# Performance work log

Hardware: AMD Instinct MI355X
Metric: run time of the kernel (lower is better)

The kernel has to match this reference:

```python
import jax, jax.numpy as jnp
import numpy as np

N = 50000      # nodes
E = 800000     # edges (avg degree 16)
D_IN, D_H, D_OUT = 128, 256, 128


def setup_inputs() -> dict:
    key = jax.random.key(0)
    ks = jax.random.split(key, 8)
    x = jax.random.normal(ks[0], (N, D_IN), dtype=jnp.float32)
    edge_index = jax.random.randint(ks[1], (2, E), 0, N, dtype=jnp.int64)
    s1 = 1.0 / np.sqrt(D_IN).astype(np.float32)
    s2 = 1.0 / np.sqrt(D_H).astype(np.float32)
    return {
        "x": x,
        "edge_index": edge_index,
        "W1l": jax.random.normal(ks[2], (D_H, D_IN), jnp.float32) * s1,
        "b1l": jnp.zeros((D_H,), jnp.float32),
        "W1r": jax.random.normal(ks[3], (D_H, D_IN), jnp.float32) * s1,
        "W2l": jax.random.normal(ks[4], (D_OUT, D_H), jnp.float32) * s2,
        "b2l": jnp.zeros((D_OUT,), jnp.float32),
        "W2r": jax.random.normal(ks[5], (D_OUT, D_H), jnp.float32) * s2,
    }


def sage_conv(x, src, dst, Wl, bl, Wr):
    # mean-aggregate source features into destination nodes
    agg = jax.ops.segment_sum(x[src], dst, num_segments=N)           # [N, d_in]
    deg = jax.ops.segment_sum(jnp.ones((src.shape[0],), x.dtype), dst, num_segments=N)
    mean = agg / jnp.maximum(deg, 1.0)[:, None]
    # lin_l(mean_agg) + lin_r(x_root); lin_r has no bias (PyG SAGEConv default)
    return mean @ Wl.T + bl + x @ Wr.T


def reference(x, edge_index, W1l, b1l, W1r, W2l, b2l, W2r):
    src, dst = edge_index[0], edge_index[1]
    h = sage_conv(x, src, dst, W1l, b1l, W1r)
    h = jax.nn.relu(h)  # dropout inactive in eval mode
    return sage_conv(h, src, dst, W2l, b2l, W2r)
```

## Files before the change

### kernel.cpp

```cpp
#include <hip/hip_runtime.h>


typedef __attribute__((ext_vector_type(8))) short bf16x8;
typedef __attribute__((ext_vector_type(4))) float floatx4;

__device__ inline unsigned short f2b(float f) {
  unsigned int x = __float_as_uint(f);
  unsigned int r = (x + 0x7fffu + ((x >> 16) & 1u)) >> 16;
  return (unsigned short)r;
}
__device__ inline float blo(unsigned int u) { return __uint_as_float(u << 16); }
__device__ inline float bhi(unsigned int u) { return __uint_as_float(u & 0xffff0000u); }

#define ACC8(A, u)                                            \
  {                                                           \
    A[0] += blo((u).x); A[1] += bhi((u).x);                   \
    A[2] += blo((u).y); A[3] += bhi((u).y);                   \
    A[4] += blo((u).z); A[5] += bhi((u).z);                   \
    A[6] += blo((u).w); A[7] += bhi((u).w);                   \
  }

__global__ void prep_kernel(const float* __restrict__ x,
                            const float* __restrict__ W1l, const float* __restrict__ W1r,
                            const float* __restrict__ W2l, const float* __restrict__ W2r,
                            unsigned short* __restrict__ Wc1, unsigned short* __restrict__ Wc2,
                            unsigned short* __restrict__ A1,
                            int* __restrict__ cnt, int* __restrict__ off, int N, int E) {
  int i = blockIdx.x * blockDim.x + threadIdx.x;
  if (i < 65536) {
    int j = i >> 8, k = i & 255;
    float v1 = (k < 128) ? W1l[j * 128 + k] : W1r[j * 128 + (k - 128)];
    Wc1[i] = f2b(v1);
    float v2 = (j < 128) ? W2l[j * 256 + k] : W2r[(j - 128) * 256 + k];
    Wc2[i] = f2b(v2);
  }
  if (i < N) cnt[i] = 0;
  if (i == 0) off[N] = E;
  if (i < N * 32) {
    int n = i >> 5, c = (i & 31) * 4;
    float4 v = *(const float4*)(x + (size_t)n * 128 + c);
    uint2 p;
    p.x = (unsigned int)f2b(v.x) | ((unsigned int)f2b(v.y) << 16);
    p.y = (unsigned int)f2b(v.z) | ((unsigned int)f2b(v.w) << 16);
    *(uint2*)(A1 + (size_t)n * 256 + 128 + c) = p;
  }
}

__global__ void hist_kernel(const int* __restrict__ dst, int* __restrict__ cnt,
                            int* __restrict__ rank, int E) {
  int i = blockIdx.x * blockDim.x + threadIdx.x;
  int e = i * 4;
  if (e + 3 < E) {
    int4 d = *(const int4*)(dst + e);
    int4 r;
    r.x = atomicAdd(&cnt[d.x], 1);
    r.y = atomicAdd(&cnt[d.y], 1);
    r.z = atomicAdd(&cnt[d.z], 1);
    r.w = atomicAdd(&cnt[d.w], 1);
    *(int4*)(rank + e) = r;
  } else {
    for (; e < E; e++) rank[e] = atomicAdd(&cnt[dst[e]], 1);
  }
}

__global__ __launch_bounds__(1024) void scan_blocks_kernel(const int* __restrict__ cnt,
                                                           int* __restrict__ off,
                                                           int* __restrict__ bsum, int N) {
  __shared__ int wsum[16];
  __shared__ int wincl[16];
  const int tid = threadIdx.x;
  const int lane = tid & 63;
  const int wv = tid >> 6;
  const int i = blockIdx.x * 1024 + tid;
  const int v = (i < N) ? cnt[i] : 0;
  int s = v;
#pragma unroll
  for (int o = 1; o < 64; o <<= 1) {
    int t = __shfl_up(s, o, 64);
    if (lane >= o) s += t;
  }
  if (lane == 63) wsum[wv] = s;
  __syncthreads();
  if (tid < 16) {
    int ws = wsum[tid];
#pragma unroll
    for (int o = 1; o < 16; o <<= 1) {
      int t = __shfl_up(ws, o, 16);
      if ((tid & 15) >= o) ws += t;
    }
    wincl[tid] = ws;
  }
  __syncthreads();
  const int wo = wv ? wincl[wv - 1] : 0;
  if (i < N) off[i] = wo + s - v;
  if (tid == 1023) bsum[blockIdx.x] = wo + s;
}

__global__ __launch_bounds__(1024) void scan_add_kernel(int* __restrict__ off,
                                                        const int* __restrict__ bsum, int N, int SB) {
  __shared__ int bofs[64];
  const int tid = threadIdx.x;
  if (tid < 64) {
    int v = (tid < SB) ? bsum[tid] : 0;
    int s = v;
#pragma unroll
    for (int o = 1; o < 64; o <<= 1) {
      int t = __shfl_up(s, o, 64);
      if (tid >= o) s += t;
    }
    bofs[tid] = s - v;
  }
  __syncthreads();
  int i = blockIdx.x * 1024 + tid;
  if (i < N) off[i] = off[i] + bofs[blockIdx.x];
}

__global__ void fill_kernel(const int* __restrict__ src, const int* __restrict__ dst,
                            const int* __restrict__ rank, const int* __restrict__ off,
                            int* __restrict__ csr, int E) {
  int i = blockIdx.x * blockDim.x + threadIdx.x;
  int e = i * 4;
  if (e + 3 < E) {
    int4 d = *(const int4*)(dst + e);
    int4 r = *(const int4*)(rank + e);
    int4 s = *(const int4*)(src + e);
    csr[off[d.x] + r.x] = s.x;
    csr[off[d.y] + r.y] = s.y;
    csr[off[d.z] + r.z] = s.z;
    csr[off[d.w] + r.w] = s.w;
  } else {
    for (; e < E; e++) csr[off[dst[e]] + rank[e]] = src[e];
  }
}

__global__ void gather1_kernel(const unsigned short* __restrict__ feat,
                               const int* __restrict__ csr, const int* __restrict__ off,
                               unsigned short* __restrict__ ob, int N) {
  int wid = (blockIdx.x * blockDim.x + threadIdx.x) >> 6;
  if (wid >= N) return;
  const int lane = threadIdx.x & 63;
  const int slot = lane >> 3;
  const int j = lane & 7;
  const int c0 = j * 8;
  const int s0 = off[wid], s1 = off[wid + 1];
  float a[16] = {};
  int e = s0 + slot;
  for (; e + 8 < s1; e += 16) {
    int i0 = csr[e], i1 = csr[e + 8];
    uint4 u0 = *(const uint4*)(feat + (size_t)i0 * 256 + c0);
    uint4 v0 = *(const uint4*)(feat + (size_t)i0 * 256 + 64 + c0);
    uint4 u1 = *(const uint4*)(feat + (size_t)i1 * 256 + c0);
    uint4 v1 = *(const uint4*)(feat + (size_t)i1 * 256 + 64 + c0);
    ACC8(a, u0); ACC8((a + 8), v0);
    ACC8(a, u1); ACC8((a + 8), v1);
  }
  for (; e < s1; e += 8) {
    int i0 = csr[e];
    uint4 u0 = *(const uint4*)(feat + (size_t)i0 * 256 + c0);
    uint4 v0 = *(const uint4*)(feat + (size_t)i0 * 256 + 64 + c0);
    ACC8(a, u0); ACC8((a + 8), v0);
  }
#pragma unroll
  for (int k = 0; k < 16; k++) {
    a[k] += __shfl_xor(a[k], 8, 64);
    a[k] += __shfl_xor(a[k], 16, 64);
    a[k] += __shfl_xor(a[k], 32, 64);
  }
  if (slot == 0) {
    const float inv = 1.0f / fmaxf((float)(s1 - s0), 1.0f);
    uint4 p;
    p.x = (unsigned int)f2b(a[0] * inv) | ((unsigned int)f2b(a[1] * inv) << 16);
    p.y = (unsigned int)f2b(a[2] * inv) | ((unsigned int)f2b(a[3] * inv) << 16);
    p.z = (unsigned int)f2b(a[4] * inv) | ((unsigned int)f2b(a[5] * inv) << 16);
    p.w = (unsigned int)f2b(a[6] * inv) | ((unsigned int)f2b(a[7] * inv) << 16);
    *(uint4*)(ob + (size_t)wid * 256 + c0) = p;
    p.x = (unsigned int)f2b(a[8] * inv) | ((unsigned int)f2b(a[9] * inv) << 16);
    p.y = (unsigned int)f2b(a[10] * inv) | ((unsigned int)f2b(a[11] * inv) << 16);
    p.z = (unsigned int)f2b(a[12] * inv) | ((unsigned int)f2b(a[13] * inv) << 16);
    p.w = (unsigned int)f2b(a[14] * inv) | ((unsigned int)f2b(a[15] * inv) << 16);
    *(uint4*)(ob + (size_t)wid * 256 + 64 + c0) = p;
  }
}

__global__ void gather2_kernel(const unsigned short* __restrict__ t,
                               const int* __restrict__ csr, const int* __restrict__ off,
                               float* __restrict__ out, int N) {
  int wid = (blockIdx.x * blockDim.x + threadIdx.x) >> 6;
  if (wid >= N) return;
  const int lane = threadIdx.x & 63;
  const int slot = lane >> 3;
  const int j = lane & 7;
  const int c0 = j * 8;
  const int s0 = off[wid], s1 = off[wid + 1];
  float a[16] = {};
  int e = s0 + slot;
  for (; e + 8 < s1; e += 16) {
    int i0 = csr[e], i1 = csr[e + 8];
    uint4 u0 = *(const uint4*)(t + (size_t)i0 * 128 + c0);
    uint4 v0 = *(const uint4*)(t + (size_t)i0 * 128 + 64 + c0);
    uint4 u1 = *(const uint4*)(t + (size_t)i1 * 128 + c0);
    uint4 v1 = *(const uint4*)(t + (size_t)i1 * 128 + 64 + c0);
    ACC8(a, u0); ACC8((a + 8), v0);
    ACC8(a, u1); ACC8((a + 8), v1);
  }
  for (; e < s1; e += 8) {
    int i0 = csr[e];
    uint4 u0 = *(const uint4*)(t + (size_t)i0 * 128 + c0);
    uint4 v0 = *(const uint4*)(t + (size_t)i0 * 128 + 64 + c0);
    ACC8(a, u0); ACC8((a + 8), v0);
  }
#pragma unroll
  for (int k = 0; k < 16; k++) {
    a[k] += __shfl_xor(a[k], 8, 64);
    a[k] += __shfl_xor(a[k], 16, 64);
    a[k] += __shfl_xor(a[k], 32, 64);
  }
  if (slot == 0) {
    const float inv = 1.0f / fmaxf((float)(s1 - s0), 1.0f);
    float4* o0 = (float4*)(out + (size_t)wid * 128 + c0);
    float4* o1 = (float4*)(out + (size_t)wid * 128 + 64 + c0);
    float4 r0 = o0[0], r1 = o0[1], r2 = o1[0], r3 = o1[1];
    r0.x += a[0] * inv;  r0.y += a[1] * inv;  r0.z += a[2] * inv;  r0.w += a[3] * inv;
    r1.x += a[4] * inv;  r1.y += a[5] * inv;  r1.z += a[6] * inv;  r1.w += a[7] * inv;
    r2.x += a[8] * inv;  r2.y += a[9] * inv;  r2.z += a[10] * inv; r2.w += a[11] * inv;
    r3.x += a[12] * inv; r3.y += a[13] * inv; r3.z += a[14] * inv; r3.w += a[15] * inv;
    o0[0] = r0; o0[1] = r1; o1[0] = r2; o1[1] = r3;
  }
}

template <int MODE>
__global__ __launch_bounds__(256, 2)
void gemm_bf16(const unsigned short* __restrict__ A, const unsigned short* __restrict__ W,
               const float* __restrict__ bias, unsigned short* __restrict__ Hout,
               float* __restrict__ Fout, int M) {
  constexpr int LDA = 72;
  __shared__ __align__(16) unsigned short As[128 * LDA];
  __shared__ __align__(16) unsigned short Ws[128 * LDA];
  const int t = threadIdx.x;
  const int lane = t & 63;
  const int wave = t >> 6;
  const int wm = (wave & 1) * 64;
  const int wn = (wave >> 1) * 64;
  const int l15 = lane & 15;
  const int quad = lane >> 4;
  const int m_blk = blockIdx.x * 128;
  const int j_blk = blockIdx.y * 128;

  floatx4 acc[4][4] = {};

  for (int kc = 0; kc < 256; kc += 64) {
    __syncthreads();
#pragma unroll
    for (int i = 0; i < 4; i++) {
      int c = t + 256 * i;
      int row = c >> 3;
      int col = (c & 7) * 8;
      int ar = m_blk + row;
      if (ar >= M) ar = M - 1;
      uint4 av = *(const uint4*)(A + (size_t)ar * 256 + kc + col);
      *(uint4*)(As + row * LDA + col) = av;
      uint4 wv = *(const uint4*)(W + (size_t)(j_blk + row) * 256 + kc + col);
      *(uint4*)(Ws + row * LDA + col) = wv;
    }
    __syncthreads();
#pragma unroll
    for (int ks = 0; ks < 64; ks += 32) {
      bf16x8 af[4], bfr[4];
#pragma unroll
      for (int mt = 0; mt < 4; mt++)
        af[mt] = *(const bf16x8*)(As + (wm + mt * 16 + l15) * LDA + ks + quad * 8);
#pragma unroll
      for (int nt = 0; nt < 4; nt++)
        bfr[nt] = *(const bf16x8*)(Ws + (wn + nt * 16 + l15) * LDA + ks + quad * 8);
#pragma unroll
      for (int mt = 0; mt < 4; mt++)
#pragma unroll
        for (int nt = 0; nt < 4; nt++)
          acc[mt][nt] = __builtin_amdgcn_mfma_f32_16x16x32_bf16(af[mt], bfr[nt], acc[mt][nt], 0, 0, 0);
    }
  }

#pragma unroll
  for (int mt = 0; mt < 4; mt++) {
#pragma unroll
    for (int nt = 0; nt < 4; nt++) {
      const int jl = wn + nt * 16 + l15;
      float bv = 0.f;
      if (MODE == 0) bv = bias[j_blk + jl];
      else if (j_blk != 0) bv = bias[jl];
#pragma unroll
      for (int r = 0; r < 4; r++) {
        const int node = m_blk + wm + mt * 16 + quad * 4 + r;
        if (node >= M) continue;
        const float v = acc[mt][nt][r];
        if (MODE == 0) {
          Hout[(size_t)node * 256 + j_blk + jl] = f2b(fmaxf(v + bv, 0.f));
        } else if (j_blk == 0) {
          Hout[(size_t)node * 128 + jl] = f2b(v);
        } else {
          Fout[(size_t)node * 128 + jl] = v + bv;
        }
      }
    }
  }
}

extern "C" void kernel_launch(void* const* d_in, const int* in_sizes, int n_in,
                              void* d_out, int out_size, void* d_ws, size_t ws_size,
                              hipStream_t stream) {
  const float* x   = (const float*)d_in[0];
  const int*  eidx = (const int*)d_in[1];
  const float* W1l = (const float*)d_in[2];
  const float* b1l = (const float*)d_in[3];
  const float* W1r = (const float*)d_in[4];
  const float* W2l = (const float*)d_in[5];
  const float* b2l = (const float*)d_in[6];
  const float* W2r = (const float*)d_in[7];
  float* out = (float*)d_out;

  const int N = in_sizes[0] / 128;
  const int E = in_sizes[1] / 2;
  const int* src = eidx;
  const int* dst = eidx + E;

  int* cnt  = (int*)d_ws;
  int* off  = cnt + N;
  int* bsum = off + N + 1;
  int* rank = bsum + 64;
  int* csr  = rank + E;
  size_t ioff = ((size_t)(N + N + 1 + 64 + 2 * E) * 4 + 15) & ~(size_t)15;
  unsigned short* A1  = (unsigned short*)((char*)d_ws + ioff);
  unsigned short* h   = A1 + (size_t)N * 256;
  unsigned short* tb  = h + (size_t)N * 256;
  unsigned short* Wc1 = tb + (size_t)N * 128;
  unsigned short* Wc2 = Wc1 + 65536;

  const int SB = (N + 1023) / 1024;

  prep_kernel<<<(N * 32 + 255) / 256, 256, 0, stream>>>(x, W1l, W1r, W2l, W2r,
                                                        Wc1, Wc2, A1, cnt, off, N, E);
  hist_kernel<<<(E / 4 + 255) / 256, 256, 0, stream>>>(dst, cnt, rank, E);
  scan_blocks_kernel<<<SB, 1024, 0, stream>>>(cnt, off, bsum, N);
  scan_add_kernel<<<SB, 1024, 0, stream>>>(off, bsum, N, SB);
  fill_kernel<<<(E / 4 + 255) / 256, 256, 0, stream>>>(src, dst, rank, off, csr, E);

  const int gblocks = (N + 3) / 4;
  gather1_kernel<<<gblocks, 256, 0, stream>>>(A1 + 128, csr, off, A1, N);

  dim3 gg((N + 127) / 128, 2);
  gemm_bf16<0><<<gg, 256, 0, stream>>>(A1, Wc1, b1l, h, nullptr, N);
  gemm_bf16<1><<<gg, 256, 0, stream>>>(h, Wc2, b2l, tb, out, N);
  gather2_kernel<<<gblocks, 256, 0, stream>>>(tb, csr, off, out, N);
}
```

Before: 276.3 us.

## Fuse both layer GEMMs into one kernel keeping hidden activations in LDS

Replaces the two separate bf16 GEMM launches with one kernel that computes a 64-row tile of the layer-1 hidden activations, keeps them in shared memory, and feeds them directly into the layer-2 GEMM. This removes the global write and re-read of the N x 256 hidden buffer and one kernel launch. In exchange, each block reloads the full weight matrices for only 64 rows, and larger LDS use (about 70KB) may reduce occupancy.

After: 272.9 us. No clear change (-1.2%).

```diff
diff --git a/kernel.cpp b/kernel.cpp
--- a/kernel.cpp
+++ b/kernel.cpp
@@ -228,77 +228,117 @@
   }
 }
 
-template <int MODE>
 __global__ __launch_bounds__(256, 2)
-void gemm_bf16(const unsigned short* __restrict__ A, const unsigned short* __restrict__ W,
-               const float* __restrict__ bias, unsigned short* __restrict__ Hout,
-               float* __restrict__ Fout, int M) {
-  constexpr int LDA = 72;
-  __shared__ __align__(16) unsigned short As[128 * LDA];
-  __shared__ __align__(16) unsigned short Ws[128 * LDA];
+void gemm_fused(const unsigned short* __restrict__ A,
+                const unsigned short* __restrict__ Wc1,
+                const unsigned short* __restrict__ Wc2,
+                const float* __restrict__ b1, const float* __restrict__ b2,
+                unsigned short* __restrict__ tb, float* __restrict__ out, int M) {
+  constexpr int LDW = 72;
+  constexpr int LDH = 264;
+  __shared__ __align__(16) unsigned short Hs[64 * LDH];
+  __shared__ __align__(16) unsigned short As[64 * LDW];
+  __shared__ __align__(16) unsigned short Ws[256 * LDW];
   const int t = threadIdx.x;
   const int lane = t & 63;
   const int wave = t >> 6;
-  const int wm = (wave & 1) * 64;
-  const int wn = (wave >> 1) * 64;
+  const int wn = wave * 64;
   const int l15 = lane & 15;
   const int quad = lane >> 4;
-  const int m_blk = blockIdx.x * 128;
-  const int j_blk = blockIdx.y * 128;
-
-  floatx4 acc[4][4] = {};
-
-  for (int kc = 0; kc < 256; kc += 64) {
-    __syncthreads();
-#pragma unroll
-    for (int i = 0; i < 4; i++) {
-      int c = t + 256 * i;
-      int row = c >> 3;
-      int col = (c & 7) * 8;
-      int ar = m_blk + row;
-      if (ar >= M) ar = M - 1;
-      uint4 av = *(const uint4*)(A + (size_t)ar * 256 + kc + col);
-      *(uint4*)(As + row * LDA + col) = av;
-      uint4 wv = *(const uint4*)(W + (size_t)(j_blk + row) * 256 + kc + col);
-      *(uint4*)(Ws + row * LDA + col) = wv;
-    }
-    __syncthreads();
-#pragma unroll
-    for (int ks = 0; ks < 64; ks += 32) {
-      bf16x8 af[4], bfr[4];
-#pragma unroll
-      for (int mt = 0; mt < 4; mt++)
-        af[mt] = *(const bf16x8*)(As + (wm + mt * 16 + l15) * LDA + ks + quad * 8);
-#pragma unroll
-      for (int nt = 0; nt < 4; nt++)
-        bfr[nt] = *(const bf16x8*)(Ws + (wn + nt * 16 + l15) * LDA + ks + quad * 8);
-#pragma unroll
-      for (int mt = 0; mt < 4; mt++)
+  const int m_blk = blockIdx.x * 64;
+
+  {
+    floatx4 acc[4][4] = {};
+    for (int kc = 0; kc < 256; kc += 64) {
+      __syncthreads();
+#pragma unroll
+      for (int i = 0; i < 2; i++) {
+        int c = t + 256 * i;
+        int row = c >> 3, col = (c & 7) * 8;
+        int ar = m_blk + row;
+        if (ar >= M) ar = M - 1;
+        *(uint4*)(As + row * LDW + col) = *(const uint4*)(A + (size_t)ar * 256 + kc + col);
+      }
+#pragma unroll
+      for (int i = 0; i < 8; i++) {
+        int c = t + 256 * i;
+        int row = c >> 3, col = (c & 7) * 8;
+        *(uint4*)(Ws + row * LDW + col) = *(const uint4*)(Wc1 + (size_t)row * 256 + kc + col);
+      }
+      __syncthreads();
+#pragma unroll
+      for (int ks = 0; ks < 64; ks += 32) {
+        bf16x8 af[4], bfr[4];
+#pragma unroll
+        for (int mt = 0; mt < 4; mt++)
+          af[mt] = *(const bf16x8*)(As + (mt * 16 + l15) * LDW + ks + quad * 8);
 #pragma unroll
         for (int nt = 0; nt < 4; nt++)
-          acc[mt][nt] = __builtin_amdgcn_mfma_f32_16x16x32_bf16(af[mt], bfr[nt], acc[mt][nt], 0, 0, 0);
-    }
-  }
-
-#pragma unroll
-  for (int mt = 0; mt < 4; mt++) {
+          bfr[nt] = *(const bf16x8*)(Ws + (wn + nt * 16 + l15) * LDW + ks + quad * 8);
+#pragma unroll
+        for (int mt = 0; mt < 4; mt++)
+#pragma unroll
+          for (int nt = 0; nt < 4; nt++)
+            acc[mt][nt] = __builtin_amdgcn_mfma_f32_16x16x32_bf16(af[mt], bfr[nt], acc[mt][nt], 0, 0, 0);
+      }
+    }
 #pragma unroll
     for (int nt = 0; nt < 4; nt++) {
       const int jl = wn + nt * 16 + l15;
-      float bv = 0.f;
-      if (MODE == 0) bv = bias[j_blk + jl];
-      else if (j_blk != 0) bv = bias[jl];
-#pragma unroll
-      for (int r = 0; r < 4; r++) {
-        const int node = m_blk + wm + mt * 16 + quad * 4 + r;
-        if (node >= M) continue;
-        const float v = acc[mt][nt][r];
-        if (MODE == 0) {
-          Hout[(size_t)node * 256 + j_blk + jl] = f2b(fmaxf(v + bv, 0.f));
-        } else if (j_blk == 0) {
-          Hout[(size_t)node * 128 + jl] = f2b(v);
-        } else {
-          Fout[(size_t)node * 128 + jl] = v + bv;
+      const float bv = b1[jl];
+#pragma unroll
+      for (int mt = 0; mt < 4; mt++) {
+#pragma unroll
+        for (int r = 0; r < 4; r++) {
+          const int row = mt * 16 + quad * 4 + r;
+          Hs[row * LDH + jl] = f2b(fmaxf(acc[mt][nt][r] + bv, 0.f));
+        }
+      }
+    }
+  }
+
+  {
+    floatx4 acc[4][4] = {};
+    for (int kc = 0; kc < 256; kc += 64) {
+      __syncthreads();
+#pragma unroll
+      for (int i = 0; i < 8; i++) {
+        int c = t + 256 * i;
+        int row = c >> 3, col = (c & 7) * 8;
+        *(uint4*)(Ws + row * LDW + col) = *(const uint4*)(Wc2 + (size_t)row * 256 + kc + col);
+      }
+      __syncthreads();
+#pragma unroll
+      for (int ks = 0; ks < 64; ks += 32) {
+        bf16x8 af[4], bfr[4];
+#pragma unroll
+        for (int mt = 0; mt < 4; mt++)
+          af[mt] = *(const bf16x8*)(Hs + (mt * 16 + l15) * LDH + kc + ks + quad * 8);
+#pragma unroll
+        for (int nt = 0; nt < 4; nt++)
+          bfr[nt] = *(const bf16x8*)(Ws + (wn + nt * 16 + l15) * LDW + ks + quad * 8);
+#pragma unroll
+        for (int mt = 0; mt < 4; mt++)
+#pragma unroll
+          for (int nt = 0; nt < 4; nt++)
+            acc[mt][nt] = __builtin_amdgcn_mfma_f32_16x16x32_bf16(af[mt], bfr[nt], acc[mt][nt], 0, 0, 0);
+      }
+    }
+#pragma unroll
+    for (int nt = 0; nt < 4; nt++) {
+      const int j = wn + nt * 16 + l15;
+#pragma unroll
+      for (int mt = 0; mt < 4; mt++) {
+#pragma unroll
+        for (int r = 0; r < 4; r++) {
+          const int node = m_blk + mt * 16 + quad * 4 + r;
+          if (node >= M) continue;
+          const float v = acc[mt][nt][r];
+          if (j < 128) {
+            tb[(size_t)node * 128 + j] = f2b(v);
+          } else {
+            out[(size_t)node * 128 + (j - 128)] = v + b2[j - 128];
+          }
         }
       }
     }
@@ -330,8 +370,7 @@
   int* csr  = rank + E;
   size_t ioff = ((size_t)(N + N + 1 + 64 + 2 * E) * 4 + 15) & ~(size_t)15;
   unsigned short* A1  = (unsigned short*)((char*)d_ws + ioff);
-  unsigned short* h   = A1 + (size_t)N * 256;
-  unsigned short* tb  = h + (size_t)N * 256;
+  unsigned short* tb  = A1 + (size_t)N * 256;
   unsigned short* Wc1 = tb + (size_t)N * 128;
   unsigned short* Wc2 = Wc1 + 65536;
 
@@ -347,8 +386,7 @@
   const int gblocks = (N + 3) / 4;
   gather1_kernel<<<gblocks, 256, 0, stream>>>(A1 + 128, csr, off, A1, N);
 
-  dim3 gg((N + 127) / 128, 2);
-  gemm_bf16<0><<<gg, 256, 0, stream>>>(A1, Wc1, b1l, h, nullptr, N);
-  gemm_bf16<1><<<gg, 256, 0, stream>>>(h, Wc2, b2l, tb, out, N);
+  gemm_fused<<<(N + 63) / 64, 256, 0, stream>>>(A1, Wc1, Wc2, b1l, b2l, tb, out, N);
+
   gather2_kernel<<<gblocks, 256, 0, stream>>>(tb, csr, off, out, N);
 }
```
